# Optimization experiments

Measured on AMD Instinct MI355X. Metric: run time of the kernel, lower is better.

Reference implementation:

```python
import jax, jax.numpy as jnp
import numpy as np

B, S, E, H, W = 4, 2048, 1024, 16, 128
HD = E // H

def setup_inputs() -> dict:
    key = jax.random.key(0)
    ks = jax.random.split(key, 5)
    scale = 1.0 / np.sqrt(E)
    x = jax.random.normal(ks[0], (B, S, E), dtype=jnp.float32)
    w_in = jax.random.uniform(ks[1], (3 * E, E), dtype=jnp.float32, minval=-scale, maxval=scale)
    b_in = jnp.zeros((3 * E,), dtype=jnp.float32)
    w_out = jax.random.uniform(ks[2], (E, E), dtype=jnp.float32, minval=-scale, maxval=scale)
    b_out = jnp.zeros((E,), dtype=jnp.float32)
    return {"x": x, "w_in": w_in, "b_in": b_in, "w_out": w_out, "b_out": b_out}

def reference(x, w_in, b_in, w_out, b_out):
    b, s, e = x.shape
    # fused QKV projection (torch MultiheadAttention in_proj)
    qkv = x @ w_in.T + b_in                      # [B,S,3E]
    q, k, v = jnp.split(qkv, 3, axis=-1)
    q = q.reshape(b, s, H, HD).transpose(0, 2, 1, 3)  # [B,H,S,HD]
    k = k.reshape(b, s, H, HD).transpose(0, 2, 1, 3)
    v = v.reshape(b, s, H, HD).transpose(0, 2, 1, 3)
    scores = jnp.einsum('bhqd,bhkd->bhqk', q, k) / jnp.sqrt(jnp.asarray(HD, x.dtype))
    # banded causal mask: row i attends to columns [i-W, i]
    i = jnp.arange(s)[:, None]
    j = jnp.arange(s)[None, :]
    allowed = (j <= i) & (j >= i - W)            # [S,S]
    scores = jnp.where(allowed[None, None], scores, jnp.asarray(-1e9, x.dtype))
    attn = jax.nn.softmax(scores, axis=-1)
    out = jnp.einsum('bhqk,bhkd->bhqd', attn, v)  # [B,H,S,HD]
    out = out.transpose(0, 2, 1, 3).reshape(b, s, e)
    return out @ w_out.T + b_out
```

## Files before the change

kernel.cpp:

```cpp
#include <hip/hip_runtime.h>
#include <stdint.h>

#define SLEN 2048
#define EMB  1024
#define NHEAD 16
#define HDIM  64
#define WINSZ 128

typedef __attribute__((ext_vector_type(8))) __bf16 bf16x8;
typedef __attribute__((ext_vector_type(4))) float  f32x4;

__device__ __forceinline__ unsigned short f2bf(float f) {
  union { float f; unsigned int u; } v;
  v.f = f;
  unsigned int r = v.u + 0x7FFFu + ((v.u >> 16) & 1u);
  return (unsigned short)(r >> 16);
}

__global__ void cvt_f32_bf16(const float* __restrict__ in, unsigned short* __restrict__ out, int n) {
  int i = (blockIdx.x * 256 + threadIdx.x) * 4;
  if (i >= n) return;
  float4 f = *(const float4*)(in + i);
  ushort4 o;
  o.x = f2bf(f.x); o.y = f2bf(f.y); o.z = f2bf(f.z); o.w = f2bf(f.w);
  *(ushort4*)(out + i) = o;
}

#define AS1(p) (const __attribute__((address_space(1))) unsigned int*)((const void*)(p))
#define AS3(p) (__attribute__((address_space(3))) unsigned int*)((void*)(p))

template <bool OUT_BF16>
__global__ __launch_bounds__(256, 2) void gemm_nt(
    const unsigned short* __restrict__ A,
    const unsigned short* __restrict__ B,
    const float* __restrict__ bias,
    void* __restrict__ Cout, int M, int N, int K)
{
  __shared__ unsigned short As[128 * 64];
  __shared__ unsigned short Bs[128 * 64];
  const int tid  = threadIdx.x;
  const int wave = tid >> 6, lane = tid & 63;
  const int quad = lane >> 4, l16 = lane & 15;
  const int wm = (wave >> 1) * 64, wn = (wave & 1) * 64;
  const long mBase = (long)blockIdx.y * 128;
  const long nBase = (long)blockIdx.x * 128;
  const int lr  = lane >> 3;
  const int lks = ((lane & 7) ^ lr) * 8;
  const int swz = l16 & 7;

  f32x4 acc[4][4];
#pragma unroll
  for (int i = 0; i < 4; ++i)
#pragma unroll
    for (int j = 0; j < 4; ++j)
#pragma unroll
      for (int r = 0; r < 4; ++r) acc[i][j][r] = 0.f;

  for (int k0 = 0; k0 < K; k0 += 64) {
    __syncthreads();
#pragma unroll
    for (int t = 0; t < 4; ++t) {
      const int r0 = (wave * 4 + t) * 8;
      const unsigned short* ga = A + (mBase + r0 + lr) * (long)K + k0 + lks;
      __builtin_amdgcn_global_load_lds(AS1(ga), AS3(As + r0 * 64), 16, 0, 0);
      const unsigned short* gb = B + (nBase + r0 + lr) * (long)K + k0 + lks;
      __builtin_amdgcn_global_load_lds(AS1(gb), AS3(Bs + r0 * 64), 16, 0, 0);
    }
    __syncthreads();

#pragma unroll
    for (int s = 0; s < 2; ++s) {
      bf16x8 aF[4], bF[4];
#pragma unroll
      for (int i = 0; i < 4; ++i)
        aF[i] = *(const bf16x8*)(As + (wm + i * 16 + l16) * 64 + (((s * 4 + quad) ^ swz) * 8));
#pragma unroll
      for (int j = 0; j < 4; ++j)
        bF[j] = *(const bf16x8*)(Bs + (wn + j * 16 + l16) * 64 + (((s * 4 + quad) ^ swz) * 8));
#pragma unroll
      for (int i = 0; i < 4; ++i)
#pragma unroll
        for (int j = 0; j < 4; ++j)
          acc[i][j] = __builtin_amdgcn_mfma_f32_16x16x32_bf16(aF[i], bF[j], acc[i][j], 0, 0, 0);
    }
  }

#pragma unroll
  for (int j = 0; j < 4; ++j) {
    const long nG = nBase + wn + j * 16 + l16;
    const float bv = bias[nG];
#pragma unroll
    for (int i = 0; i < 4; ++i)
#pragma unroll
      for (int r = 0; r < 4; ++r) {
        const long mG = mBase + wm + i * 16 + quad * 4 + r;
        const float v = acc[i][j][r] + bv;
        if (OUT_BF16) ((unsigned short*)Cout)[mG * N + nG] = f2bf(v);
        else          ((float*)Cout)[mG * N + nG] = v;
      }
  }
}

__global__ __launch_bounds__(256, 2) void local_attn(
    const unsigned short* __restrict__ qkv,
    unsigned short* __restrict__ outw)
{
  const int qb = blockIdx.x;
  const int h  = blockIdx.y;
  const int b  = blockIdx.z;
  const int tid = threadIdx.x;
  const int wave = tid >> 6, lane = tid & 63;
  const int quad = lane >> 4, l16 = lane & 15;

  __shared__ unsigned short Klds[192 * 72];
  __shared__ unsigned short Vlds[64 * 200];
  __shared__ unsigned short Plds[4][16 * 40];

  const long rowStride = 3 * EMB;
  const int kwin0 = qb * 64 - WINSZ;

  for (int c = tid; c < 192 * 8; c += 256) {
    const int key = c >> 3;
    const int dc  = (c & 7) * 8;
    const int sk  = kwin0 + key;
    uint4 val = make_uint4(0u, 0u, 0u, 0u);
    if (sk >= 0)
      val = *(const uint4*)(qkv + ((long)(b * SLEN + sk)) * rowStride + EMB + h * HDIM + dc);
    *(uint4*)(Klds + key * 72 + dc) = val;
  }
  for (int c = tid; c < 192 * 16; c += 256) {
    const int key = c >> 4;
    const int dg  = (c & 15) * 4;
    const int sk  = kwin0 + key;
    ushort4 v = make_ushort4(0, 0, 0, 0);
    if (sk >= 0)
      v = *(const ushort4*)(qkv + ((long)(b * SLEN + sk)) * rowStride + 2 * EMB + h * HDIM + dg);
    Vlds[(dg + 0) * 200 + key] = v.x;
    Vlds[(dg + 1) * 200 + key] = v.y;
    Vlds[(dg + 2) * 200 + key] = v.z;
    Vlds[(dg + 3) * 200 + key] = v.w;
  }

  const int q0 = qb * 64 + wave * 16;
  const long qrow = (long)(b * SLEN + q0 + l16) * rowStride + h * HDIM;
  const bf16x8 qA0 = *(const bf16x8*)(qkv + qrow + quad * 8);
  const bf16x8 qA1 = *(const bf16x8*)(qkv + qrow + 32 + quad * 8);

  __syncthreads();

  f32x4 Oacc[4];
  float mrow[4], lrow[4];
#pragma unroll
  for (int dt = 0; dt < 4; ++dt)
#pragma unroll
    for (int r = 0; r < 4; ++r) Oacc[dt][r] = 0.f;
#pragma unroll
  for (int r = 0; r < 4; ++r) { mrow[r] = -3.0e38f; lrow[r] = 0.f; }

  const int lbase0 = (wave * 16) & ~31;
  const float scale = 0.125f;

  for (int it = 0; it < 5; ++it) {
    const int l0 = lbase0 + it * 32;

    f32x4 sc[2];
#pragma unroll
    for (int half = 0; half < 2; ++half) {
      const int key = l0 + half * 16 + l16;
      const unsigned short* kr = Klds + key * 72;
      const bf16x8 kB0 = *(const bf16x8*)(kr + quad * 8);
      const bf16x8 kB1 = *(const bf16x8*)(kr + 32 + quad * 8);
      f32x4 s;
#pragma unroll
      for (int r = 0; r < 4; ++r) s[r] = 0.f;
      s = __builtin_amdgcn_mfma_f32_16x16x32_bf16(qA0, kB0, s, 0, 0, 0);
      s = __builtin_amdgcn_mfma_f32_16x16x32_bf16(qA1, kB1, s, 0, 0, 0);
      sc[half] = s;
    }

    float pv[2][4], rmax[4];
#pragma unroll
    for (int r = 0; r < 4; ++r) rmax[r] = -3.0e38f;
#pragma unroll
    for (int half = 0; half < 2; ++half) {
      const int kg = kwin0 + l0 + half * 16 + l16;
#pragma unroll
      for (int r = 0; r < 4; ++r) {
        const int qg = q0 + quad * 4 + r;
        float v = sc[half][r] * scale;
        const bool ok = (kg >= 0) && (kg <= qg) && (kg >= qg - WINSZ);
        v = ok ? v : -3.0e38f;
        pv[half][r] = v;
        rmax[r] = fmaxf(rmax[r], v);
      }
    }
#pragma unroll
    for (int d = 1; d < 16; d <<= 1)
#pragma unroll
      for (int r = 0; r < 4; ++r)
        rmax[r] = fmaxf(rmax[r], __shfl_xor(rmax[r], d, 64));

    float alpha[4], rsum[4];
#pragma unroll
    for (int r = 0; r < 4; ++r) {
      const float mnew = fmaxf(mrow[r], rmax[r]);
      alpha[r] = __expf(mrow[r] - mnew);
      mrow[r] = mnew;
      const float e0 = (pv[0][r] > -1.0e37f) ? __expf(pv[0][r] - mnew) : 0.f;
      const float e1 = (pv[1][r] > -1.0e37f) ? __expf(pv[1][r] - mnew) : 0.f;
      pv[0][r] = e0; pv[1][r] = e1;
      rsum[r] = e0 + e1;
    }
#pragma unroll
    for (int d = 1; d < 16; d <<= 1)
#pragma unroll
      for (int r = 0; r < 4; ++r)
        rsum[r] += __shfl_xor(rsum[r], d, 64);
#pragma unroll
    for (int r = 0; r < 4; ++r) lrow[r] = lrow[r] * alpha[r] + rsum[r];
#pragma unroll
    for (int dt = 0; dt < 4; ++dt)
#pragma unroll
      for (int r = 0; r < 4; ++r) Oacc[dt][r] *= alpha[r];

    unsigned short* P = &Plds[wave][0];
#pragma unroll
    for (int half = 0; half < 2; ++half)
#pragma unroll
      for (int r = 0; r < 4; ++r)
        P[(quad * 4 + r) * 40 + half * 16 + l16] = f2bf(pv[half][r]);
    __asm__ __volatile__("s_waitcnt lgkmcnt(0)" ::: "memory");

    const bf16x8 pA = *(const bf16x8*)(P + l16 * 40 + quad * 8);
#pragma unroll
    for (int dt = 0; dt < 4; ++dt) {
      const bf16x8 vB = *(const bf16x8*)(Vlds + (dt * 16 + l16) * 200 + l0 + quad * 8);
      Oacc[dt] = __builtin_amdgcn_mfma_f32_16x16x32_bf16(pA, vB, Oacc[dt], 0, 0, 0);
    }
  }

#pragma unroll
  for (int dt = 0; dt < 4; ++dt)
#pragma unroll
    for (int r = 0; r < 4; ++r) {
      const int qg = q0 + quad * 4 + r;
      const float v = Oacc[dt][r] / lrow[r];
      outw[(long)(b * SLEN + qg) * EMB + h * HDIM + dt * 16 + l16] = f2bf(v);
    }
}

extern "C" void kernel_launch(void* const* d_in, const int* in_sizes, int n_in,
                              void* d_out, int out_size, void* d_ws, size_t ws_size,
                              hipStream_t stream) {
  const float* x     = (const float*)d_in[0];
  const float* w_in  = (const float*)d_in[1];
  const float* b_in  = (const float*)d_in[2];
  const float* w_out = (const float*)d_in[3];
  const float* b_out = (const float*)d_in[4];
  float* out = (float*)d_out;

  char* ws = (char*)d_ws;
  unsigned short* xb    = (unsigned short*)(ws + 0);
  unsigned short* winb  = (unsigned short*)(ws + 16777216);
  unsigned short* woutb = (unsigned short*)(ws + 23068672);
  unsigned short* qkv   = (unsigned short*)(ws + 25165824);
  unsigned short* attn  = (unsigned short*)(ws + 75497472);

  const int nx = 8192 * 1024, nwin = 3072 * 1024, nwout = 1024 * 1024;
  cvt_f32_bf16<<<nx / 1024, 256, 0, stream>>>(x, xb, nx);
  cvt_f32_bf16<<<nwin / 1024, 256, 0, stream>>>(w_in, winb, nwin);
  cvt_f32_bf16<<<nwout / 1024, 256, 0, stream>>>(w_out, woutb, nwout);

  gemm_nt<true><<<dim3(3072 / 128, 8192 / 128), 256, 0, stream>>>(
      xb, winb, b_in, (void*)qkv, 8192, 3072, 1024);

  local_attn<<<dim3(SLEN / 64, NHEAD, 4), 256, 0, stream>>>(qkv, attn);

  gemm_nt<false><<<dim3(1024 / 128, 8192 / 128), 256, 0, stream>>>(
      attn, woutb, b_out, (void*)out, 8192, 1024, 1024);
}
```

Measured before the change: 231.2 us.

## Emit transposed V from QKV GEMM and restructure local attention softmax

The QKV GEMM epilogue now writes V pre-transposed into a [B,H,D,S] buffer and Q/K into a packed 2048-wide buffer. The attention kernel loads K through direct global-to-LDS loads into a swizzled layout and reads V rows with vector loads. It computes all 5 score tiles up front, so the softmax runs in a single pass instead of an online one. P is passed to the PV MFMA through cross-lane shuffles rather than an LDS round trip, and occupancy is raised to 3 blocks. The aim is to remove the scalar transposing LDS stores, the per-iteration rescaling and the shuffles. The cost is strided scattered writes in the GEMM epilogue for the V part and more live registers for the score tiles.

Result: faster. 203.8 us (-11.9%).

```diff
diff --git a/kernel.cpp b/kernel.cpp
--- a/kernel.cpp
+++ b/kernel.cpp
@@ -15,6 +15,12 @@
   v.f = f;
   unsigned int r = v.u + 0x7FFFu + ((v.u >> 16) & 1u);
   return (unsigned short)(r >> 16);
+}
+
+__device__ __forceinline__ unsigned int pack_bf(float a, float b) {
+  union { float f; unsigned int u; } x, y;
+  x.f = a; y.f = b;
+  return ((y.u + 0x8000u) & 0xFFFF0000u) | ((x.u + 0x8000u) >> 16);
 }
 
 __global__ void cvt_f32_bf16(const float* __restrict__ in, unsigned short* __restrict__ out, int n) {
@@ -29,12 +35,14 @@
 #define AS1(p) (const __attribute__((address_space(1))) unsigned int*)((const void*)(p))
 #define AS3(p) (__attribute__((address_space(3))) unsigned int*)((void*)(p))
 
-template <bool OUT_BF16>
+template <int MODE>
 __global__ __launch_bounds__(256, 2) void gemm_nt(
     const unsigned short* __restrict__ A,
     const unsigned short* __restrict__ B,
     const float* __restrict__ bias,
-    void* __restrict__ Cout, int M, int N, int K)
+    void* __restrict__ Cout,
+    unsigned short* __restrict__ vt,
+    int M, int N, int K, int ldc)
 {
   __shared__ unsigned short As[128 * 64];
   __shared__ unsigned short Bs[128 * 64];
@@ -85,24 +93,43 @@
     }
   }
 
-#pragma unroll
-  for (int j = 0; j < 4; ++j) {
-    const long nG = nBase + wn + j * 16 + l16;
-    const float bv = bias[nG];
-#pragma unroll
-    for (int i = 0; i < 4; ++i)
-#pragma unroll
-      for (int r = 0; r < 4; ++r) {
-        const long mG = mBase + wm + i * 16 + quad * 4 + r;
-        const float v = acc[i][j][r] + bv;
-        if (OUT_BF16) ((unsigned short*)Cout)[mG * N + nG] = f2bf(v);
-        else          ((float*)Cout)[mG * N + nG] = v;
-      }
-  }
-}
-
-__global__ __launch_bounds__(256, 2) void local_attn(
-    const unsigned short* __restrict__ qkv,
+  if (MODE == 1 && nBase >= 2048) {
+#pragma unroll
+    for (int j = 0; j < 4; ++j) {
+      const int nG = (int)nBase + wn + j * 16 + l16;
+      const float bv = bias[nG];
+      const int hd = nG - 2048;
+      const int hh = hd >> 6, dd = hd & 63;
+#pragma unroll
+      for (int i = 0; i < 4; ++i)
+#pragma unroll
+        for (int r = 0; r < 4; ++r) {
+          const int mG = (int)mBase + wm + i * 16 + quad * 4 + r;
+          const int bb = mG >> 11, ss = mG & 2047;
+          vt[(((long)(bb * NHEAD + hh)) * HDIM + dd) * SLEN + ss] = f2bf(acc[i][j][r] + bv);
+        }
+    }
+  } else {
+#pragma unroll
+    for (int j = 0; j < 4; ++j) {
+      const long nG = nBase + wn + j * 16 + l16;
+      const float bv = bias[nG];
+#pragma unroll
+      for (int i = 0; i < 4; ++i)
+#pragma unroll
+        for (int r = 0; r < 4; ++r) {
+          const long mG = mBase + wm + i * 16 + quad * 4 + r;
+          const float v = acc[i][j][r] + bv;
+          if (MODE == 1) ((unsigned short*)Cout)[mG * ldc + nG] = f2bf(v);
+          else           ((float*)Cout)[mG * ldc + nG] = v;
+        }
+    }
+  }
+}
+
+__global__ __launch_bounds__(256, 3) void local_attn(
+    const unsigned short* __restrict__ qk,
+    const unsigned short* __restrict__ vT,
     unsigned short* __restrict__ outw)
 {
   const int qb = blockIdx.x;
@@ -112,141 +139,135 @@
   const int wave = tid >> 6, lane = tid & 63;
   const int quad = lane >> 4, l16 = lane & 15;
 
-  __shared__ unsigned short Klds[192 * 72];
+  __shared__ unsigned short Klds[192 * 64];
   __shared__ unsigned short Vlds[64 * 200];
-  __shared__ unsigned short Plds[4][16 * 40];
-
-  const long rowStride = 3 * EMB;
+
   const int kwin0 = qb * 64 - WINSZ;
 
-  for (int c = tid; c < 192 * 8; c += 256) {
-    const int key = c >> 3;
-    const int dc  = (c & 7) * 8;
-    const int sk  = kwin0 + key;
-    uint4 val = make_uint4(0u, 0u, 0u, 0u);
-    if (sk >= 0)
-      val = *(const uint4*)(qkv + ((long)(b * SLEN + sk)) * rowStride + EMB + h * HDIM + dc);
-    *(uint4*)(Klds + key * 72 + dc) = val;
-  }
-  for (int c = tid; c < 192 * 16; c += 256) {
-    const int key = c >> 4;
-    const int dg  = (c & 15) * 4;
-    const int sk  = kwin0 + key;
-    ushort4 v = make_ushort4(0, 0, 0, 0);
-    if (sk >= 0)
-      v = *(const ushort4*)(qkv + ((long)(b * SLEN + sk)) * rowStride + 2 * EMB + h * HDIM + dg);
-    Vlds[(dg + 0) * 200 + key] = v.x;
-    Vlds[(dg + 1) * 200 + key] = v.y;
-    Vlds[(dg + 2) * 200 + key] = v.z;
-    Vlds[(dg + 3) * 200 + key] = v.w;
+  {
+    const int kr = lane >> 3, kc = lane & 7;
+    const long colOff = 1024 + h * HDIM + ((kc ^ kr) * 8);
+#pragma unroll
+    for (int t = 0; t < 6; ++t) {
+      const int u = wave * 6 + t;
+      const int sk = max(kwin0 + u * 8 + kr, 0);
+      const unsigned short* g = qk + (long)(b * SLEN + sk) * 2048 + colOff;
+      __builtin_amdgcn_global_load_lds(AS1(g), AS3(Klds + u * 512), 16, 0, 0);
+    }
+  }
+  {
+    const unsigned short* vbase = vT + ((long)(b * NHEAD + h)) * HDIM * SLEN;
+#pragma unroll
+    for (int t = 0; t < 8; ++t) {
+      const int c = t * 256 + tid;
+      const int d = c >> 5, k8 = c & 31;
+      if (k8 < 24) {
+        const int s0 = max(kwin0 + k8 * 8, 0);
+        uint4 v = *(const uint4*)(vbase + (long)d * SLEN + s0);
+        *(uint4*)(Vlds + d * 200 + k8 * 8) = v;
+      }
+    }
   }
 
   const int q0 = qb * 64 + wave * 16;
-  const long qrow = (long)(b * SLEN + q0 + l16) * rowStride + h * HDIM;
-  const bf16x8 qA0 = *(const bf16x8*)(qkv + qrow + quad * 8);
-  const bf16x8 qA1 = *(const bf16x8*)(qkv + qrow + 32 + quad * 8);
+  const long qrow = (long)(b * SLEN + q0 + l16) * 2048 + h * HDIM;
+  const bf16x8 qB0 = *(const bf16x8*)(qk + qrow + quad * 8);
+  const bf16x8 qB1 = *(const bf16x8*)(qk + qrow + 32 + quad * 8);
 
   __syncthreads();
 
+  const int lbase = (wave * 16) & ~31;
+  const int kx = l16 & 7;
+  const int a0 = (quad ^ kx) * 8;
+  const int a1 = ((4 + quad) ^ kx) * 8;
+  f32x4 sc[5][2];
+#pragma unroll
+  for (int it = 0; it < 5; ++it) {
+    const int l0 = lbase + it * 32;
+#pragma unroll
+    for (int half = 0; half < 2; ++half) {
+      const unsigned short* kr_ = Klds + (l0 + half * 16 + l16) * 64;
+      const bf16x8 kA0 = *(const bf16x8*)(kr_ + a0);
+      const bf16x8 kA1 = *(const bf16x8*)(kr_ + a1);
+      f32x4 s;
+#pragma unroll
+      for (int r = 0; r < 4; ++r) s[r] = 0.f;
+      s = __builtin_amdgcn_mfma_f32_16x16x32_bf16(kA0, qB0, s, 0, 0, 0);
+      s = __builtin_amdgcn_mfma_f32_16x16x32_bf16(kA1, qB1, s, 0, 0, 0);
+      sc[it][half] = s;
+    }
+  }
+
+  const int qlocal = WINSZ + wave * 16 + l16;
+  const int lo = max(wave * 16 + l16, kwin0 < 0 ? -kwin0 : 0);
+  const int kb = lbase + quad * 4;
+  float m = -3.0e38f;
+#pragma unroll
+  for (int it = 0; it < 5; ++it)
+#pragma unroll
+    for (int half = 0; half < 2; ++half)
+#pragma unroll
+      for (int r = 0; r < 4; ++r) {
+        const int kl = kb + it * 32 + half * 16 + r;
+        float v = sc[it][half][r] * 0.125f;
+        v = (kl >= lo && kl <= qlocal) ? v : -3.0e38f;
+        sc[it][half][r] = v;
+        m = fmaxf(m, v);
+      }
+  m = fmaxf(m, __shfl_xor(m, 16, 64));
+  m = fmaxf(m, __shfl_xor(m, 32, 64));
+
+  float lsum = 0.f;
+#pragma unroll
+  for (int it = 0; it < 5; ++it)
+#pragma unroll
+    for (int half = 0; half < 2; ++half)
+#pragma unroll
+      for (int r = 0; r < 4; ++r) {
+        const float e = __expf(sc[it][half][r] - m);
+        sc[it][half][r] = e;
+        lsum += e;
+      }
+  lsum += __shfl_xor(lsum, 16, 64);
+  lsum += __shfl_xor(lsum, 32, 64);
+  const float invl = 1.0f / lsum;
+
   f32x4 Oacc[4];
-  float mrow[4], lrow[4];
 #pragma unroll
   for (int dt = 0; dt < 4; ++dt)
 #pragma unroll
     for (int r = 0; r < 4; ++r) Oacc[dt][r] = 0.f;
-#pragma unroll
-  for (int r = 0; r < 4; ++r) { mrow[r] = -3.0e38f; lrow[r] = 0.f; }
-
-  const int lbase0 = (wave * 16) & ~31;
-  const float scale = 0.125f;
-
+
+#pragma unroll
   for (int it = 0; it < 5; ++it) {
-    const int l0 = lbase0 + it * 32;
-
-    f32x4 sc[2];
-#pragma unroll
-    for (int half = 0; half < 2; ++half) {
-      const int key = l0 + half * 16 + l16;
-      const unsigned short* kr = Klds + key * 72;
-      const bf16x8 kB0 = *(const bf16x8*)(kr + quad * 8);
-      const bf16x8 kB1 = *(const bf16x8*)(kr + 32 + quad * 8);
-      f32x4 s;
-#pragma unroll
-      for (int r = 0; r < 4; ++r) s[r] = 0.f;
-      s = __builtin_amdgcn_mfma_f32_16x16x32_bf16(qA0, kB0, s, 0, 0, 0);
-      s = __builtin_amdgcn_mfma_f32_16x16x32_bf16(qA1, kB1, s, 0, 0, 0);
-      sc[half] = s;
-    }
-
-    float pv[2][4], rmax[4];
-#pragma unroll
-    for (int r = 0; r < 4; ++r) rmax[r] = -3.0e38f;
-#pragma unroll
-    for (int half = 0; half < 2; ++half) {
-      const int kg = kwin0 + l0 + half * 16 + l16;
-#pragma unroll
-      for (int r = 0; r < 4; ++r) {
-        const int qg = q0 + quad * 4 + r;
-        float v = sc[half][r] * scale;
-        const bool ok = (kg >= 0) && (kg <= qg) && (kg >= qg - WINSZ);
-        v = ok ? v : -3.0e38f;
-        pv[half][r] = v;
-        rmax[r] = fmaxf(rmax[r], v);
-      }
-    }
-#pragma unroll
-    for (int d = 1; d < 16; d <<= 1)
-#pragma unroll
-      for (int r = 0; r < 4; ++r)
-        rmax[r] = fmaxf(rmax[r], __shfl_xor(rmax[r], d, 64));
-
-    float alpha[4], rsum[4];
+    const int l0 = lbase + it * 32;
+    const unsigned int u0 = pack_bf(sc[it][0][0], sc[it][0][1]);
+    const unsigned int u1 = pack_bf(sc[it][0][2], sc[it][0][3]);
+    const unsigned int u2 = pack_bf(sc[it][1][0], sc[it][1][1]);
+    const unsigned int u3 = pack_bf(sc[it][1][2], sc[it][1][3]);
+    unsigned int breg[4];
 #pragma unroll
     for (int r = 0; r < 4; ++r) {
-      const float mnew = fmaxf(mrow[r], rmax[r]);
-      alpha[r] = __expf(mrow[r] - mnew);
-      mrow[r] = mnew;
-      const float e0 = (pv[0][r] > -1.0e37f) ? __expf(pv[0][r] - mnew) : 0.f;
-      const float e1 = (pv[1][r] > -1.0e37f) ? __expf(pv[1][r] - mnew) : 0.f;
-      pv[0][r] = e0; pv[1][r] = e1;
-      rsum[r] = e0 + e1;
-    }
-#pragma unroll
-    for (int d = 1; d < 16; d <<= 1)
-#pragma unroll
-      for (int r = 0; r < 4; ++r)
-        rsum[r] += __shfl_xor(rsum[r], d, 64);
-#pragma unroll
-    for (int r = 0; r < 4; ++r) lrow[r] = lrow[r] * alpha[r] + rsum[r];
-#pragma unroll
-    for (int dt = 0; dt < 4; ++dt)
-#pragma unroll
-      for (int r = 0; r < 4; ++r) Oacc[dt][r] *= alpha[r];
-
-    unsigned short* P = &Plds[wave][0];
-#pragma unroll
-    for (int half = 0; half < 2; ++half)
-#pragma unroll
-      for (int r = 0; r < 4; ++r)
-        P[(quad * 4 + r) * 40 + half * 16 + l16] = f2bf(pv[half][r]);
-    __asm__ __volatile__("s_waitcnt lgkmcnt(0)" ::: "memory");
-
-    const bf16x8 pA = *(const bf16x8*)(P + l16 * 40 + quad * 8);
+      const int srcl = ((quad & 1) * 2 + (r >> 1)) * 16 + l16;
+      const unsigned int ga = __shfl((int)((r & 1) ? u1 : u0), srcl, 64);
+      const unsigned int gb = __shfl((int)((r & 1) ? u3 : u2), srcl, 64);
+      breg[r] = (quad >> 1) ? gb : ga;
+    }
+    union { unsigned int u[4]; bf16x8 v; } pB;
+    pB.u[0] = breg[0]; pB.u[1] = breg[1]; pB.u[2] = breg[2]; pB.u[3] = breg[3];
 #pragma unroll
     for (int dt = 0; dt < 4; ++dt) {
-      const bf16x8 vB = *(const bf16x8*)(Vlds + (dt * 16 + l16) * 200 + l0 + quad * 8);
-      Oacc[dt] = __builtin_amdgcn_mfma_f32_16x16x32_bf16(pA, vB, Oacc[dt], 0, 0, 0);
-    }
-  }
-
+      const bf16x8 vA = *(const bf16x8*)(Vlds + (dt * 16 + l16) * 200 + l0 + quad * 8);
+      Oacc[dt] = __builtin_amdgcn_mfma_f32_16x16x32_bf16(vA, pB.v, Oacc[dt], 0, 0, 0);
+    }
+  }
+
+  const long obase = (long)(b * SLEN + q0 + l16) * EMB + h * HDIM;
 #pragma unroll
   for (int dt = 0; dt < 4; ++dt)
 #pragma unroll
-    for (int r = 0; r < 4; ++r) {
-      const int qg = q0 + quad * 4 + r;
-      const float v = Oacc[dt][r] / lrow[r];
-      outw[(long)(b * SLEN + qg) * EMB + h * HDIM + dt * 16 + l16] = f2bf(v);
-    }
+    for (int r = 0; r < 4; ++r)
+      outw[obase + dt * 16 + quad * 4 + r] = f2bf(Oacc[dt][r] * invl);
 }
 
 extern "C" void kernel_launch(void* const* d_in, const int* in_sizes, int n_in,
@@ -263,19 +284,20 @@
   unsigned short* xb    = (unsigned short*)(ws + 0);
   unsigned short* winb  = (unsigned short*)(ws + 16777216);
   unsigned short* woutb = (unsigned short*)(ws + 23068672);
-  unsigned short* qkv   = (unsigned short*)(ws + 25165824);
-  unsigned short* attn  = (unsigned short*)(ws + 75497472);
+  unsigned short* qkb   = (unsigned short*)(ws + 25165824);
+  unsigned short* attn  = (unsigned short*)(ws + 58720256);
+  unsigned short* vT    = (unsigned short*)(ws + 75497472);
 
   const int nx = 8192 * 1024, nwin = 3072 * 1024, nwout = 1024 * 1024;
   cvt_f32_bf16<<<nx / 1024, 256, 0, stream>>>(x, xb, nx);
   cvt_f32_bf16<<<nwin / 1024, 256, 0, stream>>>(w_in, winb, nwin);
   cvt_f32_bf16<<<nwout / 1024, 256, 0, stream>>>(w_out, woutb, nwout);
 
-  gemm_nt<true><<<dim3(3072 / 128, 8192 / 128), 256, 0, stream>>>(
-      xb, winb, b_in, (void*)qkv, 8192, 3072, 1024);
-
-  local_attn<<<dim3(SLEN / 64, NHEAD, 4), 256, 0, stream>>>(qkv, attn);
-
-  gemm_nt<false><<<dim3(1024 / 128, 8192 / 128), 256, 0, stream>>>(
-      attn, woutb, b_out, (void*)out, 8192, 1024, 1024);
-}
+  gemm_nt<1><<<dim3(3072 / 128, 8192 / 128), 256, 0, stream>>>(
+      xb, winb, b_in, (void*)qkb, vT, 8192, 3072, 1024, 2048);
+
+  local_attn<<<dim3(SLEN / 64, NHEAD, 4), 256, 0, stream>>>(qkb, vT, attn);
+
+  gemm_nt<0><<<dim3(1024 / 128, 8192 / 128), 256, 0, stream>>>(
+      attn, woutb, b_out, (void*)out, nullptr, 8192, 1024, 1024, 1024);
+}
```
